# Kernel optimization log

Measured on AMD Instinct MI355X. Metric: run time of the kernel, lower is better.

## Reference

```python
import jax, jax.numpy as jnp
import numpy as np

N_MASKS, V, U = 16, 1080, 1920
FG_NUM, BG_NUM = 2048, 2048
EXPAND_RATIO = 0.2
OFFSET_MAX = 128.0


def setup_inputs() -> dict:
    key = jax.random.key(0)
    k_img, k_fg, k_bg, k_emb = jax.random.split(key, 4)
    image = jax.random.normal(k_img, (V, U, 3), dtype=jnp.float32)
    # non-empty rectangular instance masks (original code assumes nonzero masks)
    rng = np.random.RandomState(0)
    masks_np = np.zeros((N_MASKS, V, U), dtype=bool)
    for i in range(N_MASKS):
        h = rng.randint(80, 400)
        w = rng.randint(80, 600)
        v0 = rng.randint(0, V - h)
        u0 = rng.randint(0, U - w)
        masks_np[i, v0:v0 + h, u0:u0 + w] = True
    masks = jnp.asarray(masks_np)
    u_fg = jax.random.uniform(k_fg, (N_MASKS, FG_NUM), dtype=jnp.float32)
    u_bg = jax.random.uniform(k_bg, (N_MASKS, BG_NUM), dtype=jnp.float32)
    cat_emb = jax.random.normal(k_emb, (3, 3), dtype=jnp.float32)
    return {"image": image, "masks": masks, "u_fg": u_fg, "u_bg": u_bg, "cat_emb": cat_emb}


def reference(image, masks, u_fg, u_bg, cat_emb):
    n, vMax, uMax = masks.shape
    fg_num = u_fg.shape[1]
    bg_num = u_bg.shape[1]
    union = jnp.any(masks, axis=0)  # [V,U]
    # background pixels never belong to the current mask, so field there = 2*union
    cat_idx_flat = (union.astype(jnp.int32) * 2).reshape(-1)
    img_flat = image.reshape(-1, 3)
    vi = jnp.arange(vMax, dtype=jnp.int32)
    ui = jnp.arange(uMax, dtype=jnp.int32)

    def per_mask(mask, uf, ub):
        rows = jnp.any(mask, axis=1)
        cols = jnp.any(mask, axis=0)
        v0 = jnp.min(jnp.where(rows, vi, vMax))
        v1 = jnp.max(jnp.where(rows, vi, -1))
        u0 = jnp.min(jnp.where(cols, ui, uMax))
        u1 = jnp.max(jnp.where(cols, ui, -1))
        # find_expanded_coords: spans are inclusive-exclusive (v0, v1+1)
        vlen = v1 + 1 - v0
        ulen = u1 + 1 - u0
        dv = jnp.floor(EXPAND_RATIO * vlen).astype(jnp.int32)
        du = jnp.floor(EXPAND_RATIO * ulen).astype(jnp.int32)
        v0e = jnp.maximum(0, v0 - dv)
        v1e = jnp.minimum(v1 + 1 + dv, vMax - 1)
        u0e = jnp.maximum(0, u0 - du)
        u1e = jnp.minimum(u1 + 1 + du, uMax - 1)
        incrop = ((vi >= v0e) & (vi < v1e))[:, None] & ((ui >= u0e) & (ui < u1e))[None, :]
        # ---- foreground: mask pixels (mask is always inside the expanded crop) ----
        mflat = mask.reshape(-1)
        cnt_fg = jnp.sum(mflat).astype(jnp.int32)
        cs_fg = jnp.cumsum(mflat.astype(jnp.int32))
        vsum = jnp.sum(jnp.where(mask, vi[:, None].astype(jnp.float32), 0.0))
        usum = jnp.sum(jnp.where(mask, ui[None, :].astype(jnp.float32), 0.0))
        cnt_f = cnt_fg.astype(jnp.float32)
        vc = vsum / cnt_f - v0e.astype(jnp.float32)  # centroid in crop coords
        uc = usum / cnt_f - u0e.astype(jnp.float32)
        ranks_fg = jnp.minimum((uf * cnt_f).astype(jnp.int32), cnt_fg - 1)
        pos_fg = jnp.searchsorted(cs_fg, ranks_fg + 1)  # index of (r+1)-th true pixel
        vfg = (pos_fg // uMax).astype(jnp.float32)
        ufg = (pos_fg % uMax).astype(jnp.float32)
        voff = (vfg - v0e - vc) / OFFSET_MAX
        uoff = (ufg - u0e - uc) / OFFSET_MAX
        fg_pts = jnp.concatenate(
            [img_flat[pos_fg], voff[:, None], uoff[:, None], jnp.zeros((fg_num, 3), jnp.float32)], axis=1)
        # ---- background: crop pixels not in the mask ----
        bflat = (incrop & ~mask).reshape(-1)
        cnt_bg = jnp.sum(bflat).astype(jnp.int32)
        cs_bg = jnp.cumsum(bflat.astype(jnp.int32))
        ranks_bg = jnp.minimum((ub * cnt_bg.astype(jnp.float32)).astype(jnp.int32),
                               jnp.maximum(cnt_bg - 1, 0))
        pos_bg = jnp.minimum(jnp.searchsorted(cs_bg, ranks_bg + 1), vMax * uMax - 1)
        vbg = (pos_bg // uMax).astype(jnp.float32)
        ubg = (pos_bg % uMax).astype(jnp.float32)
        voffb = (vbg - v0e - vc) / OFFSET_MAX
        uoffb = (ubg - u0e - uc) / OFFSET_MAX
        bg_pts = jnp.concatenate(
            [img_flat[pos_bg], voffb[:, None], uoffb[:, None], cat_emb[cat_idx_flat[pos_bg]]], axis=1)
        bg_pts = jnp.where(cnt_bg > 0, bg_pts, 0.0)  # original leaves zeros if no bg pixels
        pts = jnp.concatenate([fg_pts, bg_pts], axis=0)
        xyxy = jnp.stack([u0 / uMax, v0 / vMax, u1 / uMax, v1 / vMax]).astype(jnp.float32)
        return pts.astype(jnp.float32), xyxy

    points, xyxys = jax.vmap(per_mask)(masks, u_fg, u_bg)
    return points, xyxys
```

## Files before the change

### kernel.cpp

```cpp
#include <hip/hip_runtime.h>
#include <math.h>

#define NM 16
#define VMAX 1080
#define UMAX 1920
#define WPR (UMAX/32)
#define FGN 2048
#define BGN 2048
#define NPT (FGN+BGN)
#define PTS_FLOATS (NM*NPT*8)
#define DET_BLOCKS 64
#define DET_WORDS (VMAX*UMAX/4)

#define OFF_FLAG    0
#define OFF_BITMAP  4096
#define OFF_ROWCNT  (OFF_BITMAP + NM*VMAX*WPR*4)
#define OFF_RUSUM   (OFF_ROWCNT + NM*VMAX*4)
#define OFF_RUMIN   (OFF_RUSUM  + NM*VMAX*4)
#define OFF_RUMAX   (OFF_RUMIN  + NM*VMAX*4)
#define OFF_PP      (OFF_RUMAX  + NM*VMAX*4)

struct SInfo {
  int v0e, v1e, u0e, u1e, cnt_fg, v0m, v1m;
  float cntf, vc, uc;
};

__device__ inline unsigned int rangemask(int widx, int a, int b) {
  int lo = widx << 5, hi = lo + 32;
  if (b <= lo || a >= hi) return 0u;
  unsigned int m = 0xFFFFFFFFu;
  if (a > lo) m &= 0xFFFFFFFFu << (a - lo);
  if (b < hi) m &= (1u << (b - lo)) - 1u;
  return m;
}

__device__ inline int u8_evidence(unsigned int x) {
  return (x & 0xFFFFFF00u) != 0u && x != 0x3F800000u;
}

__global__ __launch_bounds__(256) void k_detect(const uint4* w4, int* flag) {
  __shared__ int sev;
  if (threadIdx.x == 0) sev = 0;
  __syncthreads();
  int local = 0;
  const int nq = DET_WORDS / 4;
  for (int i = blockIdx.x * 256 + threadIdx.x; i < nq; i += DET_BLOCKS * 256) {
    uint4 x = w4[i];
    local |= u8_evidence(x.x) | u8_evidence(x.y) | u8_evidence(x.z) | u8_evidence(x.w);
  }
  if (__any(local)) { if ((threadIdx.x & 63) == 0) atomicOr(&sev, 1); }
  __syncthreads();
  if (threadIdx.x == 0) flag[blockIdx.x] = sev ? 2 : 3;
}

__device__ inline unsigned int bits4(unsigned int x) {
  unsigned int r = 0;
  r |= (x & 0x000000FFu) ? 1u : 0u;
  r |= (x & 0x0000FF00u) ? 2u : 0u;
  r |= (x & 0x00FF0000u) ? 4u : 0u;
  r |= (x & 0xFF000000u) ? 8u : 0u;
  return r;
}
__device__ inline unsigned int bits16(uint4 q) {
  return bits4(q.x) | (bits4(q.y) << 4) | (bits4(q.z) << 8) | (bits4(q.w) << 12);
}

__global__ __launch_bounds__(256) void k_rows(const void* masks, char* ws) {
  const int R = blockIdx.x * 4 + (threadIdx.x >> 6);
  const int lane = threadIdx.x & 63;
  const int n = R / VMAX, v = R % VMAX;
  int code = ((const int*)(ws + OFF_FLAG))[lane];
  for (int off = 32; off > 0; off >>= 1) code = min(code, __shfl_xor(code, off));
  const bool is_u8 = (code == 2);
  const long long base = (long long)n * VMAX * UMAX + (long long)v * UMAX;
  const int w = lane;
  unsigned int word = 0;
  if (w < WPR) {
    if (is_u8) {
      const uint4* p = (const uint4*)((const unsigned char*)masks + base) + w * 2;
      uint4 a = p[0], b = p[1];
      word = bits16(a) | (bits16(b) << 16);
    } else {
      const uint4* p = (const uint4*)((const unsigned int*)masks + base) + w * 8;
      #pragma unroll
      for (int t = 0; t < 8; t++) {
        uint4 x = p[t];
        unsigned int nib = (x.x ? 1u : 0u) | (x.y ? 2u : 0u) | (x.z ? 4u : 0u) | (x.w ? 8u : 0u);
        word |= nib << (t * 4);
      }
    }
    ((unsigned int*)(ws + OFF_BITMAP))[(long long)R * WPR + w] = word;
  }
  const int pc = __popc(word);
  int I = pc;
  for (int d = 1; d < 64; d <<= 1) { int t = __shfl_up(I, d); if (lane >= d) I += t; }
  if (w < WPR) ((int*)(ws + OFF_PP))[(long long)R * WPR + w] = I;

  int cnt = pc;
  int usum = 0, umin = 0x7FFFFFFF, umax = -1;
  if (word) {
    umin = (w << 5) + __ffs(word) - 1;
    umax = (w << 5) + 31 - __clz(word);
    int bitsum = __popc(word & 0xAAAAAAAAu)
               + 2  * __popc(word & 0xCCCCCCCCu)
               + 4  * __popc(word & 0xF0F0F0F0u)
               + 8  * __popc(word & 0xFF00FF00u)
               + 16 * __popc(word & 0xFFFF0000u);
    usum = (w << 5) * cnt + bitsum;
  }
  for (int off = 32; off > 0; off >>= 1) {
    cnt  += __shfl_xor(cnt, off);
    usum += __shfl_xor(usum, off);
    umin = min(umin, __shfl_xor(umin, off));
    umax = max(umax, __shfl_xor(umax, off));
  }
  if (lane == 0) {
    ((int*)(ws + OFF_ROWCNT))[R] = cnt;
    ((int*)(ws + OFF_RUSUM))[R] = usum;
    ((int*)(ws + OFF_RUMIN))[R] = umin;
    ((int*)(ws + OFF_RUMAX))[R] = umax;
  }
}

__global__ __launch_bounds__(256) void k_samp(const float* __restrict__ img,
                                              const float* __restrict__ ufg,
                                              const float* __restrict__ ubg,
                                              const float* __restrict__ cat,
                                              char* ws, float* __restrict__ out) {
  __shared__ int s_p[VMAX + 1];
  __shared__ int s_wt[4];
  __shared__ long long s_vs[4], s_us[4];
  __shared__ int s_cnt[4], s_v0[4], s_v1[4], s_u0[4], s_u1[4];
  __shared__ SInfo smi;
  const int n = blockIdx.x >> 4, sub = blockIdx.x & 15;
  const bool isfg = sub < 8;
  const int tid = threadIdx.x, wid = tid >> 6, lane = tid & 63;
  const int* rowcnt = (const int*)(ws + OFF_ROWCNT) + n * VMAX;
  const int* rusum  = (const int*)(ws + OFF_RUSUM)  + n * VMAX;
  const int* rumin  = (const int*)(ws + OFF_RUMIN)  + n * VMAX;
  const int* rumax  = (const int*)(ws + OFF_RUMAX)  + n * VMAX;
  const unsigned int* bmall = (const unsigned int*)(ws + OFF_BITMAP);
  const unsigned int* bmn = bmall + (long long)n * VMAX * WPR;
  const int* ppn = (const int*)(ws + OFF_PP) + (long long)n * VMAX * WPR;

  {
    int cnt = 0, v0 = 0x7FFFFFFF, v1 = -1, u0 = 0x7FFFFFFF, u1 = -1;
    long long vsum = 0, usum = 0;
    for (int v = tid; v < VMAX; v += 256) {
      int c = rowcnt[v];
      if (c > 0) { v0 = min(v0, v); v1 = max(v1, v); u0 = min(u0, rumin[v]); u1 = max(u1, rumax[v]); }
      cnt += c; vsum += (long long)c * v; usum += (long long)rusum[v];
    }
    for (int off = 32; off > 0; off >>= 1) {
      cnt  += __shfl_xor(cnt, off);
      vsum += __shfl_xor(vsum, off);
      usum += __shfl_xor(usum, off);
      v0 = min(v0, __shfl_xor(v0, off));
      v1 = max(v1, __shfl_xor(v1, off));
      u0 = min(u0, __shfl_xor(u0, off));
      u1 = max(u1, __shfl_xor(u1, off));
    }
    if (lane == 0) {
      s_cnt[wid] = cnt; s_vs[wid] = vsum; s_us[wid] = usum;
      s_v0[wid] = v0; s_v1[wid] = v1; s_u0[wid] = u0; s_u1[wid] = u1;
    }
    __syncthreads();
    if (wid == 0) {
      int c2 = (lane < 4) ? s_cnt[lane] : 0;
      long long vs2 = (lane < 4) ? s_vs[lane] : 0, us2 = (lane < 4) ? s_us[lane] : 0;
      int a0 = (lane < 4) ? s_v0[lane] : 0x7FFFFFFF, a1 = (lane < 4) ? s_v1[lane] : -1;
      int b0 = (lane < 4) ? s_u0[lane] : 0x7FFFFFFF, b1 = (lane < 4) ? s_u1[lane] : -1;
      for (int off = 1; off <= 2; off <<= 1) {
        c2 += __shfl_xor(c2, off);
        vs2 += __shfl_xor(vs2, off);
        us2 += __shfl_xor(us2, off);
        a0 = min(a0, __shfl_xor(a0, off));
        a1 = max(a1, __shfl_xor(a1, off));
        b0 = min(b0, __shfl_xor(b0, off));
        b1 = max(b1, __shfl_xor(b1, off));
      }
      if (lane == 0) {
        int vlen = a1 + 1 - a0, ulen = b1 + 1 - b0;
        int dv = (int)floorf(0.2f * (float)vlen);
        int du = (int)floorf(0.2f * (float)ulen);
        smi.v0e = max(0, a0 - dv); smi.v1e = min(a1 + 1 + dv, VMAX - 1);
        smi.u0e = max(0, b0 - du); smi.u1e = min(b1 + 1 + du, UMAX - 1);
        smi.cnt_fg = c2; smi.cntf = (float)c2;
        smi.vc = (float)((double)vs2 / (double)c2) - (float)smi.v0e;
        smi.uc = (float)((double)us2 / (double)c2) - (float)smi.u0e;
        smi.v0m = a0; smi.v1m = a1;
        if (sub == 0) {
          float* xy = out + PTS_FLOATS + n * 4;
          xy[0] = (float)b0 / (float)UMAX; xy[1] = (float)a0 / (float)VMAX;
          xy[2] = (float)b1 / (float)UMAX; xy[3] = (float)a1 / (float)VMAX;
        }
      }
    }
    __syncthreads();
  }

  {
    const int a = smi.u0e, b = smi.u1e;
    const int wlo = a >> 5, whi = (b > a) ? ((b - 1) >> 5) : wlo;
    int wbase = 0;
    for (int c = 0; c < 270; c += 64) {
      const int act = (c + lane) < 270;
      const int r = wid * 270 + c + lane;
      int s = 0;
      if (act) {
        if (isfg) {
          s = rowcnt[r];
        } else if (r >= smi.v0e && r < smi.v1e && b > a) {
          const unsigned int* row = bmn + (long long)r * WPR;
          const int* Ip = ppn + (long long)r * WPR;
          int cm;
          if (whi == wlo) {
            cm = __popc(row[wlo] & rangemask(wlo, a, b));
          } else {
            cm = __popc(row[wlo] & rangemask(wlo, a, b))
               + __popc(row[whi] & rangemask(whi, a, b))
               + (Ip[whi - 1] - Ip[wlo]);
          }
          s = (b - a) - cm;
        }
      }
      for (int d = 1; d < 64; d <<= 1) { int t = __shfl_up(s, d); if (lane >= d) s += t; }
      if (act) s_p[r + 1] = wbase + s;
      wbase += __shfl(s, 63);
    }
    if (lane == 0) s_wt[wid] = wbase;
    __syncthreads();
    int woff = 0;
    for (int k = 0; k < wid; k++) woff += s_wt[k];
    if (woff) {
      for (int c = 0; c < 270; c += 64) {
        const int act = (c + lane) < 270;
        const int r = wid * 270 + c + lane;
        if (act) s_p[r + 1] += woff;
      }
    }
    if (tid == 0) s_p[0] = 0;
    __syncthreads();
  }
  const int total = s_wt[0] + s_wt[1] + s_wt[2] + s_wt[3];

  {
    const int qi = (sub & 7) * 256 + tid;
    float r0 = 0, r1 = 0, r2 = 0, voff = 0, uoff = 0, o5 = 0, o6 = 0, o7 = 0;
    if (isfg) {
      float uf = ufg[n * FGN + qi];
      int rk = (int)(uf * smi.cntf);
      int cm = smi.cnt_fg - 1; if (rk > cm) rk = cm;
      int lo = smi.v0m, hi = smi.v1m + 1;
      while (hi - lo > 1) { int mid = (lo + hi) >> 1; if (s_p[mid] <= rk) lo = mid; else hi = mid; }
      int v = lo, rem = rk - s_p[v];
      const uint4* row4 = (const uint4*)(bmn + v * WPR);
      int w4 = rumin[v] >> 7;
      int u = 0;
      for (;; w4++) {
        uint4 x = row4[w4];
        int c0 = __popc(x.x), c1 = __popc(x.y), c2 = __popc(x.z), c3 = __popc(x.w);
        int t = c0 + c1 + c2 + c3;
        if (rem < t) {
          unsigned int word; int wi;
          if (rem < c0) { word = x.x; wi = 0; }
          else if (rem < c0 + c1) { word = x.y; wi = 1; rem -= c0; }
          else if (rem < c0 + c1 + c2) { word = x.z; wi = 2; rem -= c0 + c1; }
          else { word = x.w; wi = 3; rem -= c0 + c1 + c2; }
          while (rem--) word &= word - 1;
          u = ((w4 * 4 + wi) << 5) + __ffs(word) - 1;
          break;
        }
        rem -= t;
      }
      long long pos = (long long)v * UMAX + u;
      r0 = img[pos * 3]; r1 = img[pos * 3 + 1]; r2 = img[pos * 3 + 2];
      voff = ((float)v - (float)smi.v0e - smi.vc) * (1.0f / 128.0f);
      uoff = ((float)u - (float)smi.u0e - smi.uc) * (1.0f / 128.0f);
      float* o = out + ((long long)(n * NPT + qi)) * 8;
      o[0] = r0; o[1] = r1; o[2] = r2; o[3] = voff; o[4] = uoff; o[5] = 0.f; o[6] = 0.f; o[7] = 0.f;
    } else {
      if (total > 0) {
        float ub = ubg[n * BGN + qi];
        int rk = (int)(ub * (float)total);
        int cm = total - 1; if (rk > cm) rk = cm;
        int lo = smi.v0e, hi = smi.v1e;
        while (hi - lo > 1) { int mid = (lo + hi) >> 1; if (s_p[mid] <= rk) lo = mid; else hi = mid; }
        int v = lo, rem = rk - s_p[v];
        const uint4* row4 = (const uint4*)(bmn + v * WPR);
        const int a = smi.u0e, b = smi.u1e;
        int u = 0;
        for (int w4 = a >> 7; ; w4++) {
          uint4 x = row4[w4];
          int base = w4 << 2;
          unsigned int b0 = (~x.x) & rangemask(base + 0, a, b);
          unsigned int b1 = (~x.y) & rangemask(base + 1, a, b);
          unsigned int b2 = (~x.z) & rangemask(base + 2, a, b);
          unsigned int b3 = (~x.w) & rangemask(base + 3, a, b);
          int c0 = __popc(b0), c1 = __popc(b1), c2 = __popc(b2), c3 = __popc(b3);
          int t = c0 + c1 + c2 + c3;
          if (rem < t) {
            unsigned int word; int wi;
            if (rem < c0) { word = b0; wi = 0; }
            else if (rem < c0 + c1) { word = b1; wi = 1; rem -= c0; }
            else if (rem < c0 + c1 + c2) { word = b2; wi = 2; rem -= c0 + c1; }
            else { word = b3; wi = 3; rem -= c0 + c1 + c2; }
            while (rem--) word &= word - 1;
            u = ((base + wi) << 5) + __ffs(word) - 1;
            break;
          }
          rem -= t;
        }
        long long pos = (long long)v * UMAX + u;
        r0 = img[pos * 3]; r1 = img[pos * 3 + 1]; r2 = img[pos * 3 + 2];
        voff = ((float)v - (float)smi.v0e - smi.vc) * (1.0f / 128.0f);
        uoff = ((float)u - (float)smi.u0e - smi.uc) * (1.0f / 128.0f);
        int uni = 0, wi = u >> 5, bi = u & 31;
        #pragma unroll
        for (int k2 = 0; k2 < NM; k2++)
          uni |= (int)((bmall[((long long)k2 * VMAX + v) * WPR + wi] >> bi) & 1u);
        const float* e = cat + (uni ? 6 : 0);
        o5 = e[0]; o6 = e[1]; o7 = e[2];
      }
      float* o = out + ((long long)(n * NPT + FGN + qi)) * 8;
      o[0] = r0; o[1] = r1; o[2] = r2; o[3] = voff; o[4] = uoff; o[5] = o5; o[6] = o6; o[7] = o7;
    }
  }
}

extern "C" void kernel_launch(void* const* d_in, const int* in_sizes, int n_in,
                              void* d_out, int out_size, void* d_ws, size_t ws_size,
                              hipStream_t stream) {
  const float* img  = (const float*)d_in[0];
  const void*  masks = d_in[1];
  const float* ufg  = (const float*)d_in[2];
  const float* ubg  = (const float*)d_in[3];
  const float* cat  = (const float*)d_in[4];
  float* out = (float*)d_out;
  char* ws = (char*)d_ws;

  hipLaunchKernelGGL(k_detect, dim3(DET_BLOCKS), dim3(256), 0, stream,
                     (const uint4*)masks, (int*)(ws + OFF_FLAG));
  hipLaunchKernelGGL(k_rows, dim3(NM * VMAX / 4), dim3(256), 0, stream, masks, ws);
  hipLaunchKernelGGL(k_samp, dim3(NM * 16), dim3(256), 0, stream,
                     img, ufg, ubg, cat, ws, out);
}
```

Measured before the change: 55.76 us.

## Drop per-row word prefix sums and double sampling blocks per mask

Removes the per-word popcount prefix-sum scan and its workspace store from the row kernel. The background row-count step now popcounts the crop's words directly with uint4 loads instead of reading that prefix array. The sampling kernel launches twice as many blocks, each handling 128 points with half its threads idle in the sampling phase. This spreads the work across more CUs, but every block still repeats the per-mask reduction and row prefix scan, so that redundant work doubles.

Result: slower. 60.23 us (+8.0%).

```diff
diff --git a/kernel.cpp b/kernel.cpp
--- a/kernel.cpp
+++ b/kernel.cpp
@@ -18,7 +18,6 @@
 #define OFF_RUSUM   (OFF_ROWCNT + NM*VMAX*4)
 #define OFF_RUMIN   (OFF_RUSUM  + NM*VMAX*4)
 #define OFF_RUMAX   (OFF_RUMIN  + NM*VMAX*4)
-#define OFF_PP      (OFF_RUMAX  + NM*VMAX*4)
 
 struct SInfo {
   int v0e, v1e, u0e, u1e, cnt_fg, v0m, v1m;
@@ -91,12 +90,7 @@
     }
     ((unsigned int*)(ws + OFF_BITMAP))[(long long)R * WPR + w] = word;
   }
-  const int pc = __popc(word);
-  int I = pc;
-  for (int d = 1; d < 64; d <<= 1) { int t = __shfl_up(I, d); if (lane >= d) I += t; }
-  if (w < WPR) ((int*)(ws + OFF_PP))[(long long)R * WPR + w] = I;
-
-  int cnt = pc;
+  int cnt = __popc(word);
   int usum = 0, umin = 0x7FFFFFFF, umax = -1;
   if (word) {
     umin = (w << 5) + __ffs(word) - 1;
@@ -132,8 +126,8 @@
   __shared__ long long s_vs[4], s_us[4];
   __shared__ int s_cnt[4], s_v0[4], s_v1[4], s_u0[4], s_u1[4];
   __shared__ SInfo smi;
-  const int n = blockIdx.x >> 4, sub = blockIdx.x & 15;
-  const bool isfg = sub < 8;
+  const int n = blockIdx.x >> 5, sub = blockIdx.x & 31;
+  const bool isfg = sub < 16;
   const int tid = threadIdx.x, wid = tid >> 6, lane = tid & 63;
   const int* rowcnt = (const int*)(ws + OFF_ROWCNT) + n * VMAX;
   const int* rusum  = (const int*)(ws + OFF_RUSUM)  + n * VMAX;
@@ -141,7 +135,6 @@
   const int* rumax  = (const int*)(ws + OFF_RUMAX)  + n * VMAX;
   const unsigned int* bmall = (const unsigned int*)(ws + OFF_BITMAP);
   const unsigned int* bmn = bmall + (long long)n * VMAX * WPR;
-  const int* ppn = (const int*)(ws + OFF_PP) + (long long)n * VMAX * WPR;
 
   {
     int cnt = 0, v0 = 0x7FFFFFFF, v1 = -1, u0 = 0x7FFFFFFF, u1 = -1;
@@ -201,7 +194,6 @@
 
   {
     const int a = smi.u0e, b = smi.u1e;
-    const int wlo = a >> 5, whi = (b > a) ? ((b - 1) >> 5) : wlo;
     int wbase = 0;
     for (int c = 0; c < 270; c += 64) {
       const int act = (c + lane) < 270;
@@ -211,15 +203,16 @@
         if (isfg) {
           s = rowcnt[r];
         } else if (r >= smi.v0e && r < smi.v1e && b > a) {
-          const unsigned int* row = bmn + (long long)r * WPR;
-          const int* Ip = ppn + (long long)r * WPR;
-          int cm;
-          if (whi == wlo) {
-            cm = __popc(row[wlo] & rangemask(wlo, a, b));
-          } else {
-            cm = __popc(row[wlo] & rangemask(wlo, a, b))
-               + __popc(row[whi] & rangemask(whi, a, b))
-               + (Ip[whi - 1] - Ip[wlo]);
+          const uint4* r4 = (const uint4*)(bmn + (long long)r * WPR);
+          const int wlo = a >> 5, whi = (b - 1) >> 5;
+          int cm = 0;
+          for (int w4 = wlo >> 2; w4 <= (whi >> 2); w4++) {
+            uint4 x = r4[w4];
+            int base2 = w4 << 2;
+            cm += __popc(x.x & rangemask(base2 + 0, a, b));
+            cm += __popc(x.y & rangemask(base2 + 1, a, b));
+            cm += __popc(x.z & rangemask(base2 + 2, a, b));
+            cm += __popc(x.w & rangemask(base2 + 3, a, b));
           }
           s = (b - a) - cm;
         }
@@ -244,8 +237,8 @@
   }
   const int total = s_wt[0] + s_wt[1] + s_wt[2] + s_wt[3];
 
-  {
-    const int qi = (sub & 7) * 256 + tid;
+  if (tid < 128) {
+    const int qi = (sub & 15) * 128 + tid;
     float r0 = 0, r1 = 0, r2 = 0, voff = 0, uoff = 0, o5 = 0, o6 = 0, o7 = 0;
     if (isfg) {
       float uf = ufg[n * FGN + qi];
@@ -342,6 +335,6 @@
   hipLaunchKernelGGL(k_detect, dim3(DET_BLOCKS), dim3(256), 0, stream,
                      (const uint4*)masks, (int*)(ws + OFF_FLAG));
   hipLaunchKernelGGL(k_rows, dim3(NM * VMAX / 4), dim3(256), 0, stream, masks, ws);
-  hipLaunchKernelGGL(k_samp, dim3(NM * 16), dim3(256), 0, stream,
+  hipLaunchKernelGGL(k_samp, dim3(NM * 32), dim3(256), 0, stream,
                      img, ufg, ubg, cat, ws, out);
 }
```
